# Optimization experiments

Hardware: AMD Instinct MI355X
Metric: run time of the kernel (lower is better)

## Reference

```python
import jax, jax.numpy as jnp
import numpy as np
from functools import partial

N = 100000
E = 1600000
F_IN, F_HID, F_OUT = 128, 128, 64


def setup_inputs() -> dict:
    key = jax.random.key(0)
    ks = jax.random.split(key, 10)
    x = jax.random.normal(ks[0], (N, F_IN), dtype=jnp.float32)
    edge_index = jax.random.randint(ks[1], (2, E), 0, N, dtype=jnp.int64)
    edge_attr = jax.random.uniform(ks[2], (E,), dtype=jnp.float32)
    # GCNConv params: Linear(in, out, bias=False) weight + separate bias
    def glorot(k, fan_in, fan_out):
        lim = jnp.sqrt(6.0 / (fan_in + fan_out))
        return jax.random.uniform(k, (fan_in, fan_out), minval=-lim, maxval=lim, dtype=jnp.float32)
    return {
        "x": x, "edge_index": edge_index, "edge_attr": edge_attr,
        "W1": glorot(ks[3], F_IN, F_HID),  "b1": jnp.zeros((F_HID,), jnp.float32),
        "W2": glorot(ks[4], F_HID, F_HID), "b2": jnp.zeros((F_HID,), jnp.float32),
        "W3": glorot(ks[5], F_HID, F_OUT), "b3": jnp.zeros((F_OUT,), jnp.float32),
    }


def _gcn_norm(src, dst, ew, n):
    # PyG gcn_norm: add self-loops with weight 1, symmetric normalization.
    loop = jnp.arange(n, dtype=src.dtype)
    src_f = jnp.concatenate([src, loop])
    dst_f = jnp.concatenate([dst, loop])
    ew_f = jnp.concatenate([ew, jnp.ones((n,), ew.dtype)])
    deg = jax.ops.segment_sum(ew_f, dst_f, num_segments=n)
    dinv = jnp.where(deg > 0, jax.lax.rsqrt(deg), 0.0)
    norm = dinv[src_f] * ew_f * dinv[dst_f]  # [E+N]
    return src_f, dst_f, norm


def _gcn_conv(x, W, b, src_f, dst_f, norm, n):
    h = x @ W  # [N, out]
    msg = norm[:, None] * h[src_f]  # gather + per-edge scale
    out = jax.ops.segment_sum(msg, dst_f, num_segments=n)  # scatter-add
    return out + b


def reference(x, edge_index, edge_attr, W1, b1, W2, b2, W3, b3):
    n = x.shape[0]
    src, dst = edge_index[0], edge_index[1]
    src_f, dst_f, norm = _gcn_norm(src, dst, edge_attr, n)
    h = jax.nn.relu(_gcn_conv(x, W1, b1, src_f, dst_f, norm, n))
    h = jax.nn.relu(_gcn_conv(h, W2, b2, src_f, dst_f, norm, n))
    out = _gcn_conv(h, W3, b3, src_f, dst_f, norm, n)
    return jax.nn.log_softmax(out, axis=-1)
```

## Files before the change

kernel.cpp:

```cpp
#include <hip/hip_runtime.h>

typedef unsigned short ushortT;
typedef unsigned int uintT;
typedef unsigned long long ullT;
typedef __attribute__((ext_vector_type(8))) short bf16x8;
typedef __attribute__((ext_vector_type(4))) float f32x4;

#define NBUCK 391
#define EPB   4096
#define NBEB  391
#define BSLOT 4608

union H16 { ushortT u; _Float16 h; };

__device__ __forceinline__ float bf2f(uintT u16) {
    return __uint_as_float(u16 << 16);
}
__device__ __forceinline__ ushortT f2bf(float f) {
    unsigned int u = __float_as_uint(f);
    unsigned int r = (u + 0x7fffu + ((u >> 16) & 1u)) >> 16;
    return (ushortT)r;
}


__device__ __forceinline__ void twist_body(const float* W, ushortT* Wt, int K, int C, int idx) {
    if (idx < K * C) {
        int k = idx / C, c = idx - k * C;
        Wt[c * K + k] = f2bf(W[idx]);
    }
}

template <int C, bool ABF16>
__device__ __forceinline__ void gemm_body(const void* Aop, const ushortT* Wt,
                                          ushortT* outp, int nrows, int bid, int tid) {
    const int K = 128;
    int wv = tid >> 6;
    int ln = tid & 63;
    int row0 = (bid * 4 + wv) * 16;
    if (row0 >= nrows) return;
    int rA = ln & 15;
    int kg = ln >> 4;
    int rowA = row0 + rA;
    bool okA = rowA < nrows;

    bf16x8 af[4];
    if (ABF16) {
        const ushortT* A = (const ushortT*)Aop;
        #pragma unroll
        for (int kb = 0; kb < 4; ++kb) {
            if (okA) af[kb] = *(const bf16x8*)(A + (size_t)rowA * K + kb * 32 + kg * 8);
            else     af[kb] = (bf16x8)(short)0;
        }
    } else {
        const float* A = (const float*)Aop;
        #pragma unroll
        for (int kb = 0; kb < 4; ++kb) {
            bf16x8 t = (bf16x8)(short)0;
            if (okA) {
                const float4* ap = reinterpret_cast<const float4*>(A + (size_t)rowA * K + kb * 32 + kg * 8);
                float4 p0 = ap[0], p1 = ap[1];
                t[0] = (short)f2bf(p0.x); t[1] = (short)f2bf(p0.y);
                t[2] = (short)f2bf(p0.z); t[3] = (short)f2bf(p0.w);
                t[4] = (short)f2bf(p1.x); t[5] = (short)f2bf(p1.y);
                t[6] = (short)f2bf(p1.z); t[7] = (short)f2bf(p1.w);
            }
            af[kb] = t;
        }
    }

    int colB = ln & 15;
    f32x4 acc[C / 16];
    #pragma unroll
    for (int nt = 0; nt < C / 16; ++nt) acc[nt] = (f32x4)0.0f;
    #pragma unroll
    for (int nt = 0; nt < C / 16; ++nt) {
        int c = nt * 16 + colB;
        #pragma unroll
        for (int kb = 0; kb < 4; ++kb) {
            bf16x8 bfr = *(const bf16x8*)(Wt + c * K + kb * 32 + kg * 8);
            acc[nt] = __builtin_amdgcn_mfma_f32_16x16x32_bf16(af[kb], bfr, acc[nt], 0, 0, 0);
        }
    }
    #pragma unroll
    for (int nt = 0; nt < C / 16; ++nt) {
        #pragma unroll
        for (int r = 0; r < 4; ++r) {
            int rowC = row0 + (ln >> 4) * 4 + r;
            if (rowC < nrows) outp[(size_t)rowC * C + nt * 16 + colB] = f2bf(acc[nt][r]);
        }
    }
}

__global__ __launch_bounds__(512) void k_sort_twist(const int* src, const int* dst, const float* ew,
                                                    int* bucket_count, ullT* erec, int e,
                                                    const float* W1, ushortT* Wt1,
                                                    const float* W2, ushortT* Wt2,
                                                    const float* W3, ushortT* Wt3) {
    __shared__ ullT srec[EPB];
    __shared__ int  gaddr[EPB];
    __shared__ int  hist[512];
    __shared__ int  adj[NBUCK];
    int blk = blockIdx.x, t = threadIdx.x;
    if (blk >= NBEB) {
        int tb = blk - NBEB;
        if (tb < 32)      twist_body(W1, Wt1, 128, 128, tb * 512 + t);
        else if (tb < 64) twist_body(W2, Wt2, 128, 128, (tb - 32) * 512 + t);
        else              twist_body(W3, Wt3, 128, 64, (tb - 64) * 512 + t);
        return;
    }
    hist[t] = 0;
    __syncthreads();
    int base = blk * EPB;
    for (int j = t; j < EPB; j += 512) {
        int i = base + j;
        if (i < e) atomicAdd(&hist[dst[i] >> 8], 1);
    }
    __syncthreads();
    int myc = hist[t];
    for (int off = 1; off < 512; off <<= 1) {
        int x = 0; if (t >= off) x = hist[t - off];
        __syncthreads();
        if (t >= off) hist[t] += x;
        __syncthreads();
    }
    int lb = (t == 0) ? 0 : hist[t - 1];
    __syncthreads();
    hist[t] = lb;
    if (t < NBUCK) {
        int gb = 0;
        if (myc > 0) gb = atomicAdd(&bucket_count[t], myc);
        adj[t] = t * BSLOT + gb - lb;
    }
    __syncthreads();
    for (int j = t; j < EPB; j += 512) {
        int i = base + j;
        if (i < e) {
            int d = dst[i];
            int b = d >> 8;
            int pos = atomicAdd(&hist[b], 1);
            H16 cv; cv.h = (_Float16)ew[i];
            ullT rec = ((ullT)(uintT)src[i] << 24) | ((ullT)(uintT)(d & 255) << 16) | (ullT)cv.u;
            srec[pos] = rec;
            int ga = adj[b] + pos;
            int lim = b * BSLOT + BSLOT - 1;
            gaddr[pos] = ga <= lim ? ga : lim;
        }
    }
    __syncthreads();
    int m = e - base; if (m > EPB) m = EPB;
    for (int k = t; k < m; k += 512) {
        erec[(size_t)gaddr[k]] = srec[k];
    }
}

__global__ __launch_bounds__(256) void k_bucket_gemm1(const ullT* erec,
                                                      const int* bucket_count,
                                                      uintT* entries, float* dinv, int* counts, int n,
                                                      const float* x, const ushortT* Wt1,
                                                      ushortT* hw1) {
    __shared__ int cnt[256];
    __shared__ uintT wsum[256];
    int blk = blockIdx.x, t = threadIdx.x;
    if (blk < NBUCK) {
        int b = blk;
        cnt[t] = 0; wsum[t] = 0;
        __syncthreads();
        int beg = b * BSLOT, m = bucket_count[b];
        if (m > BSLOT) m = BSLOT;
        for (int j = t; j < m; j += 256) {
            ullT rec = erec[(size_t)beg + j];
            int dlow = (int)((rec >> 16) & 255);
            ushortT hu = (ushortT)(rec & 0xffffu);
            int slot = atomicAdd(&cnt[dlow], 1);
            H16 cv; cv.u = hu;
            atomicAdd(&wsum[dlow], (uintT)__float2uint_rn((float)cv.h * 16777216.0f));
            if (slot < 64) {
                uintT s = (uintT)(rec >> 24);
                entries[((size_t)b * 256 + dlow) * 64 + slot] = (s << 15) | (uintT)hu;
            }
        }
        __syncthreads();
        int node = b * 256 + t;
        if (node < n) {
            float sum = (float)wsum[t] * (1.0f / 16777216.0f);
            dinv[node] = rsqrtf(1.0f + sum);
            int c = cnt[t];
            counts[node] = c > 64 ? 64 : c;
        }
    } else {
        gemm_body<128, false>(x, Wt1, hw1, n, blk - NBUCK, t);
    }
}

template <int C, bool ABF16>
__global__ __launch_bounds__(256) void k_gemm(const void* Aop, const ushortT* Wt,
                                              ushortT* outp, int nrows) {
    gemm_body<C, ABF16>(Aop, Wt, outp, nrows, blockIdx.x, threadIdx.x);
}

__global__ __launch_bounds__(256) void k_agg128(const char* hwb, const float* dinv,
                                                const int* counts, const uintT* entries,
                                                const float* bias, uintT* outp, int n) {
    __shared__ ullT wp[4][64];
    int wv = threadIdx.x >> 6, ln = threadIdx.x & 63;
    int i = blockIdx.x * 4 + wv;
    if (i >= n) return;

    float wfac = dinv[i];
    int cnt = counts[i];
    int cntp = (cnt + 7) & ~7;
    uintT ent = entries[(size_t)i * 64 + ln];
    int s_l = (ln < cnt) ? (int)(ent >> 15) : 0;
    H16 cv; cv.u = (ushortT)(ent & 0x7fffu);
    float w_l = (ln < cnt) ? dinv[s_l] * (float)cv.h * wfac : 0.f;
    wp[wv][ln] = ((ullT)__float_as_uint(w_l) << 32) | (ullT)((uintT)s_l << 8);

    const char* lane_base = hwb + (size_t)ln * 4;
    uintT us = *(const uintT*)(lane_base + (size_t)i * 256);
    float selfw = wfac * wfac;
    float acc0 = selfw * bf2f(us & 0xffffu);
    float acc1 = selfw * bf2f(us >> 16);

    for (int e = 0; e < cntp; e += 8) {
        ullT p0 = wp[wv][e + 0], p1 = wp[wv][e + 1], p2 = wp[wv][e + 2], p3 = wp[wv][e + 3];
        ullT p4 = wp[wv][e + 4], p5 = wp[wv][e + 5], p6 = wp[wv][e + 6], p7 = wp[wv][e + 7];
        uintT u0 = *(const uintT*)(lane_base + (uintT)p0);
        uintT u1 = *(const uintT*)(lane_base + (uintT)p1);
        uintT u2 = *(const uintT*)(lane_base + (uintT)p2);
        uintT u3 = *(const uintT*)(lane_base + (uintT)p3);
        uintT u4 = *(const uintT*)(lane_base + (uintT)p4);
        uintT u5 = *(const uintT*)(lane_base + (uintT)p5);
        uintT u6 = *(const uintT*)(lane_base + (uintT)p6);
        uintT u7 = *(const uintT*)(lane_base + (uintT)p7);
        float w0 = __uint_as_float((uintT)(p0 >> 32)), w1 = __uint_as_float((uintT)(p1 >> 32));
        float w2 = __uint_as_float((uintT)(p2 >> 32)), w3 = __uint_as_float((uintT)(p3 >> 32));
        float w4 = __uint_as_float((uintT)(p4 >> 32)), w5 = __uint_as_float((uintT)(p5 >> 32));
        float w6 = __uint_as_float((uintT)(p6 >> 32)), w7 = __uint_as_float((uintT)(p7 >> 32));
        acc0 += w0 * bf2f(u0 & 0xffffu); acc1 += w0 * bf2f(u0 >> 16);
        acc0 += w1 * bf2f(u1 & 0xffffu); acc1 += w1 * bf2f(u1 >> 16);
        acc0 += w2 * bf2f(u2 & 0xffffu); acc1 += w2 * bf2f(u2 >> 16);
        acc0 += w3 * bf2f(u3 & 0xffffu); acc1 += w3 * bf2f(u3 >> 16);
        acc0 += w4 * bf2f(u4 & 0xffffu); acc1 += w4 * bf2f(u4 >> 16);
        acc0 += w5 * bf2f(u5 & 0xffffu); acc1 += w5 * bf2f(u5 >> 16);
        acc0 += w6 * bf2f(u6 & 0xffffu); acc1 += w6 * bf2f(u6 >> 16);
        acc0 += w7 * bf2f(u7 & 0xffffu); acc1 += w7 * bf2f(u7 >> 16);
    }
    float2 bs = *(const float2*)(bias + 2 * ln);
    acc0 = fmaxf(acc0 + bs.x, 0.f);
    acc1 = fmaxf(acc1 + bs.y, 0.f);
    outp[(size_t)i * 64 + ln] = (uintT)f2bf(acc0) | ((uintT)f2bf(acc1) << 16);
}

__global__ __launch_bounds__(256) void k_agg_softmax(const char* hwb, const float* dinv,
                                                     const int* counts, const uintT* entries,
                                                     const float* bias, float* outp, int n) {
    __shared__ ullT wp[4][64];
    int wv = threadIdx.x >> 6, ln = threadIdx.x & 63;
    int i = blockIdx.x * 4 + wv;
    if (i >= n) return;

    float wfac = dinv[i];
    int cnt = counts[i];
    int cntp = (cnt + 7) & ~7;
    uintT ent = entries[(size_t)i * 64 + ln];
    int s_l = (ln < cnt) ? (int)(ent >> 15) : 0;
    H16 cv; cv.u = (ushortT)(ent & 0x7fffu);
    float w_l = (ln < cnt) ? dinv[s_l] * (float)cv.h * wfac : 0.f;
    wp[wv][ln] = ((ullT)__float_as_uint(w_l) << 32) | (ullT)((uintT)s_l << 7);

    const char* lane_base = hwb + (size_t)ln * 2;
    H16 sv; sv.u = *(const ushortT*)(lane_base + (size_t)i * 128);
    float acc = wfac * wfac * bf2f(sv.u);

    for (int e = 0; e < cntp; e += 8) {
        ullT p0 = wp[wv][e + 0], p1 = wp[wv][e + 1], p2 = wp[wv][e + 2], p3 = wp[wv][e + 3];
        ullT p4 = wp[wv][e + 4], p5 = wp[wv][e + 5], p6 = wp[wv][e + 6], p7 = wp[wv][e + 7];
        ushortT h0 = *(const ushortT*)(lane_base + (uintT)p0);
        ushortT h1 = *(const ushortT*)(lane_base + (uintT)p1);
        ushortT h2 = *(const ushortT*)(lane_base + (uintT)p2);
        ushortT h3 = *(const ushortT*)(lane_base + (uintT)p3);
        ushortT h4 = *(const ushortT*)(lane_base + (uintT)p4);
        ushortT h5 = *(const ushortT*)(lane_base + (uintT)p5);
        ushortT h6 = *(const ushortT*)(lane_base + (uintT)p6);
        ushortT h7 = *(const ushortT*)(lane_base + (uintT)p7);
        acc += __uint_as_float((uintT)(p0 >> 32)) * bf2f(h0);
        acc += __uint_as_float((uintT)(p1 >> 32)) * bf2f(h1);
        acc += __uint_as_float((uintT)(p2 >> 32)) * bf2f(h2);
        acc += __uint_as_float((uintT)(p3 >> 32)) * bf2f(h3);
        acc += __uint_as_float((uintT)(p4 >> 32)) * bf2f(h4);
        acc += __uint_as_float((uintT)(p5 >> 32)) * bf2f(h5);
        acc += __uint_as_float((uintT)(p6 >> 32)) * bf2f(h6);
        acc += __uint_as_float((uintT)(p7 >> 32)) * bf2f(h7);
    }
    acc += bias[ln];
    float m = acc;
    #pragma unroll
    for (int off = 32; off; off >>= 1) m = fmaxf(m, __shfl_xor(m, off));
    float ex = __expf(acc - m);
    float sm = ex;
    #pragma unroll
    for (int off = 32; off; off >>= 1) sm += __shfl_xor(sm, off);
    float r = acc - m - __logf(sm);
    outp[(size_t)i * 64 + ln] = r;
}

extern "C" void kernel_launch(void* const* d_in, const int* in_sizes, int n_in,
                              void* d_out, int out_size, void* d_ws, size_t ws_size,
                              hipStream_t stream) {
    const int N = 100000, E = 1600000;
    const int NPAD = NBUCK * 256;
    const float* x  = (const float*)d_in[0];
    const int*   src = (const int*)d_in[1];
    const int*   dst = src + E;
    const float* ea = (const float*)d_in[2];
    const float* W1 = (const float*)d_in[3];
    const float* b1 = (const float*)d_in[4];
    const float* W2 = (const float*)d_in[5];
    const float* b2 = (const float*)d_in[6];
    const float* W3 = (const float*)d_in[7];
    const float* b3 = (const float*)d_in[8];
    float* outp = (float*)d_out;

    char* ws = (char*)d_ws;
    auto alloc = [&](size_t bytes) {
        char* p = ws;
        ws += (bytes + 255) & ~(size_t)255;
        return p;
    };
    int*   bucket_count = (int*)alloc((size_t)NBUCK * 4);
    ullT*  erec         = (ullT*)alloc((size_t)NBUCK * BSLOT * 8);
    float* dinv    = (float*)alloc((size_t)N * 4);
    int*   counts  = (int*)  alloc((size_t)N * 4);
    uintT* entries = (uintT*)alloc((size_t)NPAD * 64 * 4);
    ushortT* Wt1   = (ushortT*)alloc(128 * 128 * 2);
    ushortT* Wt2   = (ushortT*)alloc(128 * 128 * 2);
    ushortT* Wt3   = (ushortT*)alloc(128 * 64 * 2);
    ushortT* hwA   = (ushortT*)alloc((size_t)N * 128 * 2);
    ushortT* hwB   = (ushortT*)alloc((size_t)N * 128 * 2);

    const int nbGemm = (N + 63) / 64;
    const int nbAgg  = (N + 3) / 4;

    hipMemsetAsync(bucket_count, 0, (size_t)NBUCK * 4, stream);
    k_sort_twist<<<NBEB + 80, 512, 0, stream>>>(src, dst, ea, bucket_count, erec, E,
                                                W1, Wt1, W2, Wt2, W3, Wt3);
    k_bucket_gemm1<<<NBUCK + nbGemm, 256, 0, stream>>>(erec, bucket_count,
                                                       entries, dinv, counts, N,
                                                       x, Wt1, hwA);
    k_agg128<<<nbAgg, 256, 0, stream>>>((const char*)hwA, dinv, counts, entries,
                                        b1, (uintT*)hwB, N);
    k_gemm<128, true><<<nbGemm, 256, 0, stream>>>(hwB, Wt2, hwA, N);
    k_agg128<<<nbAgg, 256, 0, stream>>>((const char*)hwA, dinv, counts, entries,
                                        b2, (uintT*)hwB, N);
    k_gemm<64, true><<<nbGemm, 256, 0, stream>>>(hwB, Wt3, hwA, N);
    k_agg_softmax<<<nbAgg, 256, 0, stream>>>((const char*)hwA, dinv, counts, entries,
                                             b3, outp, N);
}
```

Before: 407.1 us.

## Split aggregation wavefront into edge groups with 16-byte gathers and lane reduction

The gather-aggregate kernels are restructured so each lane loads 16 bytes (8 bf16 features) per neighbor row. Sub-groups of the wavefront handle different edges in parallel and are then combined with cross-lane shuffles. Loads are software-pipelined one iteration ahead, and the log-softmax reduction is adapted to 8 values per lane. The aim is fewer, wider memory transactions and more memory-level parallelism per wave, at the cost of extra shuffle reductions and more registers.

```diff
diff --git a/kernel.cpp b/kernel.cpp
--- a/kernel.cpp
+++ b/kernel.cpp
@@ -16,11 +16,23 @@
 __device__ __forceinline__ float bf2f(uintT u16) {
     return __uint_as_float(u16 << 16);
 }
+__device__ __forceinline__ float bflo(uintT u) {
+    return __uint_as_float(u << 16);
+}
+__device__ __forceinline__ float bfhi(uintT u) {
+    return __uint_as_float(u & 0xffff0000u);
+}
 __device__ __forceinline__ ushortT f2bf(float f) {
     unsigned int u = __float_as_uint(f);
     unsigned int r = (u + 0x7fffu + ((u >> 16) & 1u)) >> 16;
     return (ushortT)r;
 }
+
+#define ACC8(U, W) \
+    acc[0] = fmaf(W, bflo(U.x), acc[0]); acc[1] = fmaf(W, bfhi(U.x), acc[1]); \
+    acc[2] = fmaf(W, bflo(U.y), acc[2]); acc[3] = fmaf(W, bfhi(U.y), acc[3]); \
+    acc[4] = fmaf(W, bflo(U.z), acc[4]); acc[5] = fmaf(W, bfhi(U.z), acc[5]); \
+    acc[6] = fmaf(W, bflo(U.w), acc[6]); acc[7] = fmaf(W, bfhi(U.w), acc[7]);
 
 
 __device__ __forceinline__ void twist_body(const float* W, ushortT* Wt, int K, int C, int idx) {
@@ -205,6 +217,8 @@
     int wv = threadIdx.x >> 6, ln = threadIdx.x & 63;
     int i = blockIdx.x * 4 + wv;
     if (i >= n) return;
+    int lg = ln & 15;
+    int gp = ln >> 4;
 
     float wfac = dinv[i];
     int cnt = counts[i];
@@ -214,41 +228,49 @@
     H16 cv; cv.u = (ushortT)(ent & 0x7fffu);
     float w_l = (ln < cnt) ? dinv[s_l] * (float)cv.h * wfac : 0.f;
     wp[wv][ln] = ((ullT)__float_as_uint(w_l) << 32) | (ullT)((uintT)s_l << 8);
-
-    const char* lane_base = hwb + (size_t)ln * 4;
-    uintT us = *(const uintT*)(lane_base + (size_t)i * 256);
+    const ullT* wpw = wp[wv];
+
+    const char* lane_base = hwb + (size_t)(lg * 16);
+    uint4 uself = *(const uint4*)(lane_base + (size_t)i * 256);
+
+    float acc[8];
+    #pragma unroll
+    for (int j = 0; j < 8; ++j) acc[j] = 0.f;
+
+    ullT pa = wpw[gp], pb = wpw[4 + gp];
+    uint4 ua = *(const uint4*)(lane_base + (uintT)pa);
+    uint4 ub = *(const uint4*)(lane_base + (uintT)pb);
+    for (int e = 8; e < cntp; e += 8) {
+        ullT pa2 = wpw[e + gp], pb2 = wpw[e + 4 + gp];
+        uint4 ua2 = *(const uint4*)(lane_base + (uintT)pa2);
+        uint4 ub2 = *(const uint4*)(lane_base + (uintT)pb2);
+        float wa = __uint_as_float((uintT)(pa >> 32));
+        float wb = __uint_as_float((uintT)(pb >> 32));
+        ACC8(ua, wa)
+        ACC8(ub, wb)
+        pa = pa2; pb = pb2; ua = ua2; ub = ub2;
+    }
+    {
+        float wa = __uint_as_float((uintT)(pa >> 32));
+        float wb = __uint_as_float((uintT)(pb >> 32));
+        ACC8(ua, wa)
+        ACC8(ub, wb)
+    }
+
+    #pragma unroll
+    for (int j = 0; j < 8; ++j) {
+        acc[j] += __shfl_xor(acc[j], 16);
+        acc[j] += __shfl_xor(acc[j], 32);
+    }
     float selfw = wfac * wfac;
-    float acc0 = selfw * bf2f(us & 0xffffu);
-    float acc1 = selfw * bf2f(us >> 16);
-
-    for (int e = 0; e < cntp; e += 8) {
-        ullT p0 = wp[wv][e + 0], p1 = wp[wv][e + 1], p2 = wp[wv][e + 2], p3 = wp[wv][e + 3];
-        ullT p4 = wp[wv][e + 4], p5 = wp[wv][e + 5], p6 = wp[wv][e + 6], p7 = wp[wv][e + 7];
-        uintT u0 = *(const uintT*)(lane_base + (uintT)p0);
-        uintT u1 = *(const uintT*)(lane_base + (uintT)p1);
-        uintT u2 = *(const uintT*)(lane_base + (uintT)p2);
-        uintT u3 = *(const uintT*)(lane_base + (uintT)p3);
-        uintT u4 = *(const uintT*)(lane_base + (uintT)p4);
-        uintT u5 = *(const uintT*)(lane_base + (uintT)p5);
-        uintT u6 = *(const uintT*)(lane_base + (uintT)p6);
-        uintT u7 = *(const uintT*)(lane_base + (uintT)p7);
-        float w0 = __uint_as_float((uintT)(p0 >> 32)), w1 = __uint_as_float((uintT)(p1 >> 32));
-        float w2 = __uint_as_float((uintT)(p2 >> 32)), w3 = __uint_as_float((uintT)(p3 >> 32));
-        float w4 = __uint_as_float((uintT)(p4 >> 32)), w5 = __uint_as_float((uintT)(p5 >> 32));
-        float w6 = __uint_as_float((uintT)(p6 >> 32)), w7 = __uint_as_float((uintT)(p7 >> 32));
-        acc0 += w0 * bf2f(u0 & 0xffffu); acc1 += w0 * bf2f(u0 >> 16);
-        acc0 += w1 * bf2f(u1 & 0xffffu); acc1 += w1 * bf2f(u1 >> 16);
-        acc0 += w2 * bf2f(u2 & 0xffffu); acc1 += w2 * bf2f(u2 >> 16);
-        acc0 += w3 * bf2f(u3 & 0xffffu); acc1 += w3 * bf2f(u3 >> 16);
-        acc0 += w4 * bf2f(u4 & 0xffffu); acc1 += w4 * bf2f(u4 >> 16);
-        acc0 += w5 * bf2f(u5 & 0xffffu); acc1 += w5 * bf2f(u5 >> 16);
-        acc0 += w6 * bf2f(u6 & 0xffffu); acc1 += w6 * bf2f(u6 >> 16);
-        acc0 += w7 * bf2f(u7 & 0xffffu); acc1 += w7 * bf2f(u7 >> 16);
-    }
-    float2 bs = *(const float2*)(bias + 2 * ln);
-    acc0 = fmaxf(acc0 + bs.x, 0.f);
-    acc1 = fmaxf(acc1 + bs.y, 0.f);
-    outp[(size_t)i * 64 + ln] = (uintT)f2bf(acc0) | ((uintT)f2bf(acc1) << 16);
+    ACC8(uself, selfw)
+
+    float a0 = (gp & 1) ? ((gp & 2) ? acc[6] : acc[2]) : ((gp & 2) ? acc[4] : acc[0]);
+    float a1 = (gp & 1) ? ((gp & 2) ? acc[7] : acc[3]) : ((gp & 2) ? acc[5] : acc[1]);
+    float2 bs = *(const float2*)(bias + (lg * 8 + gp * 2));
+    a0 = fmaxf(a0 + bs.x, 0.f);
+    a1 = fmaxf(a1 + bs.y, 0.f);
+    outp[(size_t)i * 64 + (lg * 4 + gp)] = (uintT)f2bf(a0) | ((uintT)f2bf(a1) << 16);
 }
 
 __global__ __launch_bounds__(256) void k_agg_softmax(const char* hwb, const float* dinv,
@@ -258,6 +280,8 @@
     int wv = threadIdx.x >> 6, ln = threadIdx.x & 63;
     int i = blockIdx.x * 4 + wv;
     if (i >= n) return;
+    int lg = ln & 7;
+    int gp = ln >> 3;
 
     float wfac = dinv[i];
     int cnt = counts[i];
@@ -267,41 +291,65 @@
     H16 cv; cv.u = (ushortT)(ent & 0x7fffu);
     float w_l = (ln < cnt) ? dinv[s_l] * (float)cv.h * wfac : 0.f;
     wp[wv][ln] = ((ullT)__float_as_uint(w_l) << 32) | (ullT)((uintT)s_l << 7);
-
-    const char* lane_base = hwb + (size_t)ln * 2;
-    H16 sv; sv.u = *(const ushortT*)(lane_base + (size_t)i * 128);
-    float acc = wfac * wfac * bf2f(sv.u);
-
-    for (int e = 0; e < cntp; e += 8) {
-        ullT p0 = wp[wv][e + 0], p1 = wp[wv][e + 1], p2 = wp[wv][e + 2], p3 = wp[wv][e + 3];
-        ullT p4 = wp[wv][e + 4], p5 = wp[wv][e + 5], p6 = wp[wv][e + 6], p7 = wp[wv][e + 7];
-        ushortT h0 = *(const ushortT*)(lane_base + (uintT)p0);
-        ushortT h1 = *(const ushortT*)(lane_base + (uintT)p1);
-        ushortT h2 = *(const ushortT*)(lane_base + (uintT)p2);
-        ushortT h3 = *(const ushortT*)(lane_base + (uintT)p3);
-        ushortT h4 = *(const ushortT*)(lane_base + (uintT)p4);
-        ushortT h5 = *(const ushortT*)(lane_base + (uintT)p5);
-        ushortT h6 = *(const ushortT*)(lane_base + (uintT)p6);
-        ushortT h7 = *(const ushortT*)(lane_base + (uintT)p7);
-        acc += __uint_as_float((uintT)(p0 >> 32)) * bf2f(h0);
-        acc += __uint_as_float((uintT)(p1 >> 32)) * bf2f(h1);
-        acc += __uint_as_float((uintT)(p2 >> 32)) * bf2f(h2);
-        acc += __uint_as_float((uintT)(p3 >> 32)) * bf2f(h3);
-        acc += __uint_as_float((uintT)(p4 >> 32)) * bf2f(h4);
-        acc += __uint_as_float((uintT)(p5 >> 32)) * bf2f(h5);
-        acc += __uint_as_float((uintT)(p6 >> 32)) * bf2f(h6);
-        acc += __uint_as_float((uintT)(p7 >> 32)) * bf2f(h7);
-    }
-    acc += bias[ln];
-    float m = acc;
-    #pragma unroll
-    for (int off = 32; off; off >>= 1) m = fmaxf(m, __shfl_xor(m, off));
-    float ex = __expf(acc - m);
-    float sm = ex;
-    #pragma unroll
-    for (int off = 32; off; off >>= 1) sm += __shfl_xor(sm, off);
-    float r = acc - m - __logf(sm);
-    outp[(size_t)i * 64 + ln] = r;
+    const ullT* wpw = wp[wv];
+
+    const char* lane_base = hwb + (size_t)(lg * 16);
+    uint4 uself = *(const uint4*)(lane_base + (size_t)i * 128);
+
+    float acc[8];
+    #pragma unroll
+    for (int j = 0; j < 8; ++j) acc[j] = 0.f;
+
+    ullT pa = wpw[gp];
+    uint4 ua = *(const uint4*)(lane_base + (uintT)pa);
+    for (int e = 8; e < cntp; e += 8) {
+        ullT pa2 = wpw[e + gp];
+        uint4 ua2 = *(const uint4*)(lane_base + (uintT)pa2);
+        float wa = __uint_as_float((uintT)(pa >> 32));
+        ACC8(ua, wa)
+        pa = pa2; ua = ua2;
+    }
+    {
+        float wa = __uint_as_float((uintT)(pa >> 32));
+        ACC8(ua, wa)
+    }
+
+    #pragma unroll
+    for (int j = 0; j < 8; ++j) {
+        acc[j] += __shfl_xor(acc[j], 8);
+        acc[j] += __shfl_xor(acc[j], 16);
+        acc[j] += __shfl_xor(acc[j], 32);
+    }
+    float selfw = wfac * wfac;
+    ACC8(uself, selfw)
+
+    float4 bsa = *(const float4*)(bias + lg * 8);
+    float4 bsb = *(const float4*)(bias + lg * 8 + 4);
+    acc[0] += bsa.x; acc[1] += bsa.y; acc[2] += bsa.z; acc[3] += bsa.w;
+    acc[4] += bsb.x; acc[5] += bsb.y; acc[6] += bsb.z; acc[7] += bsb.w;
+
+    float m = acc[0];
+    #pragma unroll
+    for (int j = 1; j < 8; ++j) m = fmaxf(m, acc[j]);
+    m = fmaxf(m, __shfl_xor(m, 1));
+    m = fmaxf(m, __shfl_xor(m, 2));
+    m = fmaxf(m, __shfl_xor(m, 4));
+    float s = 0.f;
+    #pragma unroll
+    for (int j = 0; j < 8; ++j) s += __expf(acc[j] - m);
+    s += __shfl_xor(s, 1);
+    s += __shfl_xor(s, 2);
+    s += __shfl_xor(s, 4);
+    float ls = m + __logf(s);
+
+    float v0 = (gp & 1) ? acc[4] : acc[0];
+    float v1 = (gp & 1) ? acc[5] : acc[1];
+    float v2 = (gp & 1) ? acc[6] : acc[2];
+    float v3 = (gp & 1) ? acc[7] : acc[3];
+    if (gp < 2) {
+        float4 r = { v0 - ls, v1 - ls, v2 - ls, v3 - ls };
+        *(float4*)(outp + (size_t)i * 64 + lg * 8 + gp * 4) = r;
+    }
 }
 
 extern "C" void kernel_launch(void* const* d_in, const int* in_sizes, int n_in,
```

Result: no change. 405.6 us (-0.4%).
